# Performance work log

Hardware: AMD Instinct MI355X
Metric: run time of the kernel (lower is better)

## Reference

```python
import jax, jax.numpy as jnp
import numpy as np

BN_EPS = 1e-5

def _bn_relu(x, gamma, beta):
    # training-mode BatchNorm1d: biased batch stats over (B, N) per channel
    mean = x.mean(axis=(0, 2), keepdims=True)
    var = x.var(axis=(0, 2), keepdims=True)
    xn = (x - mean) * jax.lax.rsqrt(var + BN_EPS)
    return jax.nn.relu(xn * gamma[None, :, None] + beta[None, :, None])


def setup_inputs() -> dict:
    key = jax.random.key(0)
    ks = jax.random.split(key, 12)
    B, n1, n2, c1, c2 = 16, 4096, 1024, 128, 256
    in_ch, mlp = c1 + c2, [256, 128]
    xyz1 = jax.random.uniform(ks[0], (B, n1, 3), dtype=jnp.float32)
    xyz2 = jax.random.uniform(ks[1], (B, n2, 3), dtype=jnp.float32)
    feat1 = jax.random.normal(ks[2], (B, c1, n1), dtype=jnp.float32)
    feat2 = jax.random.normal(ks[3], (B, c2, n2), dtype=jnp.float32)
    # Conv1d(k=1) weights as (out, in) matrices; kaiming-ish scale
    w0 = jax.random.normal(ks[4], (mlp[0], in_ch), dtype=jnp.float32) / np.sqrt(in_ch)
    b0 = jnp.zeros((mlp[0],), jnp.float32)
    g0 = jnp.ones((mlp[0],), jnp.float32)
    be0 = jnp.zeros((mlp[0],), jnp.float32)
    w1 = jax.random.normal(ks[5], (mlp[1], mlp[0]), dtype=jnp.float32) / np.sqrt(mlp[0])
    b1 = jnp.zeros((mlp[1],), jnp.float32)
    g1 = jnp.ones((mlp[1],), jnp.float32)
    be1 = jnp.zeros((mlp[1],), jnp.float32)
    return {"xyz1": xyz1, "xyz2": xyz2, "feat1": feat1, "feat2": feat2,
            "w0": w0, "b0": b0, "g0": g0, "be0": be0,
            "w1": w1, "b1": b1, "g1": g1, "be1": be1}


def reference(xyz1, xyz2, feat1, feat2, w0, b0, g0, be0, w1, b1, g1, be1):
    # three_nn_interpolate: squared pairwise dists (B, n1, n2)
    d = jnp.sum((xyz1[:, :, None, :] - xyz2[:, None, :, :]) ** 2, axis=-1)
    neg_d3, idx3 = jax.lax.top_k(-d, 3)          # 3 smallest dists
    d3 = -neg_d3                                  # (B, n1, 3)
    w = 1.0 / (d3 + 1e-8)
    w = w / jnp.sum(w, axis=-1, keepdims=True)
    # gather feat2 at knn indices: (B, c2, n1, 3)
    gathered = jnp.take_along_axis(feat2[:, :, None, :], idx3[:, None, :, :], axis=3)
    interp = jnp.sum(gathered * w[:, None, :, :], axis=-1)  # (B, c2, n1)

    x = jnp.concatenate([feat1, interp], axis=1)            # (B, c1+c2, n1)
    x = _bn_relu(jnp.einsum('oc,bcn->bon', w0, x) + b0[None, :, None], g0, be0)
    x = _bn_relu(jnp.einsum('oc,bcn->bon', w1, x) + b1[None, :, None], g1, be1)
    return x
```

## Files before the change

kernel.cpp:

```cpp
#include <hip/hip_runtime.h>
#include <hip/hip_bf16.h>

typedef unsigned short u16;
typedef __attribute__((ext_vector_type(8))) __bf16 bf16x8;
typedef __attribute__((ext_vector_type(4))) float floatx4;

#define B_   16
#define N1_  4096
#define N2_  1024
#define C1_  128
#define C2_  256
#define CIN_ 384
#define CM_  256
#define CO_  128

__device__ __forceinline__ u16 f2bf(float f) {
  unsigned u = __float_as_uint(f);
  u = (u + 0x7fffu + ((u >> 16) & 1u)) >> 16;
  return (u16)u;
}
__device__ __forceinline__ float bf2f(u16 h) {
  return __uint_as_float(((unsigned)h) << 16);
}

union U128 { uint4 u; bf16x8 v; u16 s[8]; };

__device__ __forceinline__ bf16x8 ldfrag(const u16* p) {
  U128 x; x.u = *(const uint4*)p; return x.v;
}
__device__ __forceinline__ uint4 pack8(const u16* h) {
  uint4 u;
  u.x = (unsigned)h[0] | ((unsigned)h[1] << 16);
  u.y = (unsigned)h[2] | ((unsigned)h[3] << 16);
  u.z = (unsigned)h[4] | ((unsigned)h[5] << 16);
  u.w = (unsigned)h[6] | ((unsigned)h[7] << 16);
  return u;
}


__global__ __launch_bounds__(256) void mega_kernel(
    const float* __restrict__ xyz1, const float* __restrict__ xyz2,
    float* __restrict__ pd, int* __restrict__ pi,
    const float* __restrict__ w0, const float* __restrict__ w1,
    u16* __restrict__ w0b, u16* __restrict__ w1b,
    const float* __restrict__ feat2, u16* __restrict__ feat2Tb,
    const float* __restrict__ feat1, u16* __restrict__ xcatT)
{
  __shared__ __align__(16) float smem[64*133];
  int t = threadIdx.x;
  int id = blockIdx.x;
  if (id < 2048) {
    float4* sp = (float4*)smem;
    int xb = id & 15, b = (id >> 4) & 15, chunk = id >> 8;
    const float* p2 = xyz2 + ((size_t)b * N2_ + chunk * 128) * 3;
    if (t < 128) sp[t] = make_float4(p2[t*3], p2[t*3+1], p2[t*3+2], 0.f);
    __syncthreads();
    int i = xb * 256 + t;
    const float* p1 = xyz1 + ((size_t)b * N1_ + i) * 3;
    float x = p1[0], y = p1[1], z = p1[2];
    float d0 = 1e30f, d1 = 1e30f, d2 = 1e30f;
    int i0 = 0, i1 = 0, i2 = 0;
    int jb = chunk * 128;
    #pragma unroll 4
    for (int j = 0; j < 128; ++j) {
      float4 p = sp[j];
      float dx = x - p.x, dy = y - p.y, dz = z - p.z;
      float d = dx*dx + dy*dy + dz*dz;
      if (d < d2) {
        int jj = jb + j;
        if (d < d0)      { d2=d1; i2=i1; d1=d0; i1=i0; d0=d; i0=jj; }
        else if (d < d1) { d2=d1; i2=i1; d1=d;  i1=jj; }
        else             { d2=d;  i2=jj; }
      }
    }
    int o = chunk*65536 + b*4096 + i;
    pd[o] = d0; pd[o + 524288] = d1; pd[o + 1048576] = d2;
    pi[o] = i0; pi[o + 524288] = i1; pi[o + 1048576] = i2;
    return;
  }
  if (id < 2176) {
    int item = (id - 2048) * 256 + t;
    if (item < 12288) {
      int m = item / 48, kc = item % 48;
      const float* p = w0 + m * CIN_ + kc * 8;
      u16 h8[8];
      #pragma unroll
      for (int j = 0; j < 8; ++j) h8[j] = f2bf(p[j]);
      int mt = m >> 4, col = m & 15, kt = kc >> 2, quad = kc & 3;
      *(uint4*)(w0b + ((mt*12 + kt)*512 + (quad*16 + col)*8)) = pack8(h8);
    } else if (item < 16384) {
      int i2 = item - 12288;
      int m = i2 >> 5, kc = i2 & 31;
      const float* p = w1 + m * CM_ + kc * 8;
      u16 h8[8];
      #pragma unroll
      for (int j = 0; j < 8; ++j) h8[j] = f2bf(p[j]);
      int mt = m >> 4, col = m & 15, kt = kc >> 2, quad = kc & 3;
      *(uint4*)(w1b + ((mt*8 + kt)*512 + (quad*16 + col)*8)) = pack8(h8);
    }
    return;
  }
  if (id < 2432) {
    float (*sA2)[129] = (float(*)[129])smem;
    int idx = id - 2176;
    int b = idx >> 4, n0 = (idx & 15) * 64;
    #pragma unroll 1
    for (int h = 0; h < 2; ++h) {
      if (h) __syncthreads();
      #pragma unroll
      for (int j = 0; j < 8; ++j) {
        int flat4 = t + j * 256;
        int cl = flat4 >> 4, nn4 = (flat4 & 15) * 4;
        float4 v = *(const float4*)(feat2 + ((size_t)b*C2_ + h*128 + cl)*N2_ + n0 + nn4);
        sA2[nn4+0][cl] = v.x; sA2[nn4+1][cl] = v.y; sA2[nn4+2][cl] = v.z; sA2[nn4+3][cl] = v.w;
      }
      __syncthreads();
      int nn = t & 63, chunk = t >> 6;
      u16* dst = feat2Tb + ((size_t)b*N2_ + n0 + nn)*C2_ + h*128 + chunk*32;
      #pragma unroll
      for (int g = 0; g < 4; ++g) {
        u16 h8[8];
        #pragma unroll
        for (int j = 0; j < 8; ++j) h8[j] = f2bf(sA2[nn][chunk*32 + g*8 + j]);
        *(uint4*)(dst + g*8) = pack8(h8);
      }
    }
    return;
  }
  {
    float (*sA1)[133] = (float(*)[133])smem;
    int idx = id - 2432;
    int b = idx >> 6, n0 = (idx & 63) * 64;
    #pragma unroll
    for (int j = 0; j < 8; ++j) {
      int flat4 = t + j * 256;
      int c = flat4 >> 4, nn4 = (flat4 & 15) * 4;
      float4 v = *(const float4*)(feat1 + ((size_t)b*C1_ + c)*N1_ + n0 + nn4);
      sA1[nn4+0][c] = v.x; sA1[nn4+1][c] = v.y; sA1[nn4+2][c] = v.z; sA1[nn4+3][c] = v.w;
    }
    __syncthreads();
    int nn = t & 63, chunk = t >> 6;
    int n = n0 + nn, nt = n >> 4, col = n & 15;
    u16* tb = xcatT + ((size_t)b*256 + nt)*12*512;
    #pragma unroll
    for (int g = 0; g < 4; ++g) {
      int c0 = chunk*32 + g*8;
      u16 h8[8];
      #pragma unroll
      for (int j = 0; j < 8; ++j) h8[j] = f2bf(sA1[nn][c0 + j]);
      *(uint4*)(tb + (size_t)chunk*512 + (g*16 + col)*8) = pack8(h8);
    }
  }
}

__global__ __launch_bounds__(256) void merge_kernel(
    const float* __restrict__ pd, const int* __restrict__ pi,
    int* __restrict__ idx_out, float* __restrict__ w_out)
{
  int p = blockIdx.x * 256 + threadIdx.x;
  float d0 = 1e30f, d1 = 1e30f, d2 = 1e30f;
  int i0 = 0, i1 = 0, i2 = 0;
  #pragma unroll
  for (int c = 0; c < 8; ++c) {
    int o = c*65536 + p;
    #pragma unroll
    for (int k = 0; k < 3; ++k) {
      float d = pd[o + k*524288];
      int ix = pi[o + k*524288];
      bool c2 = d < d2, c1 = d < d1, c0 = d < d0;
      d2 = c1 ? d1 : (c2 ? d  : d2);
      i2 = c1 ? i1 : (c2 ? ix : i2);
      d1 = c0 ? d0 : (c1 ? d  : d1);
      i1 = c0 ? i0 : (c1 ? ix : i1);
      d0 = c0 ? d  : d0;
      i0 = c0 ? ix : i0;
    }
  }
  float w0 = 1.f/(d0+1e-8f), w1 = 1.f/(d1+1e-8f), w2 = 1.f/(d2+1e-8f);
  float inv = 1.f/(w0+w1+w2);
  idx_out[p]          = i0;
  idx_out[p +  65536] = i1;
  idx_out[p + 131072] = i2;
  w_out[p]            = w0*inv;
  w_out[p +  65536]   = w1*inv;
  w_out[p + 131072]   = w2*inv;
}

__global__ __launch_bounds__(256) void interp_kernel(
    const u16* __restrict__ feat2Tb,
    const int* __restrict__ idx_in, const float* __restrict__ w_in,
    u16* __restrict__ xcatT)
{
  int b = blockIdx.y;
  int t = threadIdx.x;
  int p0 = blockIdx.x * 64;
  int seg = t & 31;
  int pl  = t >> 5;
  #pragma unroll 2
  for (int pass = 0; pass < 8; ++pass) {
    int n = p0 + pass*8 + pl;
    int base = b*N1_ + n;
    int i0 = idx_in[base], i1 = idx_in[base + 65536], i2 = idx_in[base + 131072];
    float w0 = w_in[base], w1 = w_in[base + 65536], w2 = w_in[base + 131072];
    const u16* fb = feat2Tb + (size_t)b*N2_*C2_ + seg*8;
    U128 a, c, d;
    a.u = *(const uint4*)(fb + (size_t)i0*C2_);
    c.u = *(const uint4*)(fb + (size_t)i1*C2_);
    d.u = *(const uint4*)(fb + (size_t)i2*C2_);
    u16 h8[8];
    #pragma unroll
    for (int j = 0; j < 8; ++j)
      h8[j] = f2bf(w0*bf2f(a.s[j]) + w1*bf2f(c.s[j]) + w2*bf2f(d.s[j]));
    int nt = n >> 4, col = n & 15;
    int kt = 4 + (seg >> 2), quad = seg & 3;
    *(uint4*)(xcatT + (((size_t)b*256 + nt)*12 + kt)*512 + (quad*16 + col)*8) = pack8(h8);
  }
}

__global__ __launch_bounds__(256) void gemm1_mfma(
    const u16* __restrict__ xcatT, const u16* __restrict__ w0b,
    const float* __restrict__ b0p, u16* __restrict__ y0T,
    float* __restrict__ p0)
{
  __shared__ float ps[4][64][2];
  int t = threadIdx.x;
  int wave = t >> 6, lane = t & 63;
  int col = lane & 15, quad = lane >> 4;
  int wm = wave >> 1, wn = wave & 1;
  int b = blockIdx.y;
  int mtb = blockIdx.z*8 + wm*4;
  int ntb = blockIdx.x*8 + wn*4;

  const u16* ap = w0b + lane*8;
  const u16* bp = xcatT + ((size_t)(b*256 + ntb)*12)*512 + lane*8;

  floatx4 acc[4][4] = {};
  bf16x8 aA[4], aB[4], aC[4], aD[4], bA[4], bB[4], bC[4], bD[4];

#define G1_LDA(BUF, KT) { _Pragma("unroll") for (int i = 0; i < 4; ++i) \
    BUF[i] = ldfrag(ap + (size_t)((mtb+i)*12 + (KT))*512); }
#define G1_LDB(BUF, KT) { _Pragma("unroll") for (int i = 0; i < 4; ++i) \
    BUF[i] = ldfrag(bp + (size_t)(i*12 + (KT))*512); }
#define G1_MM(A_, B_) { _Pragma("unroll") for (int mt = 0; mt < 4; ++mt) \
    _Pragma("unroll") for (int nt = 0; nt < 4; ++nt) \
      acc[mt][nt] = __builtin_amdgcn_mfma_f32_16x16x32_bf16(A_[mt], B_[nt], acc[mt][nt], 0, 0, 0); }

  G1_LDA(aA,0);  G1_LDB(bA,0);
  G1_LDA(aB,1);  G1_LDB(bB,1);
  G1_LDA(aC,2);  G1_LDB(bC,2);
  G1_LDA(aD,3);  G1_LDB(bD,3);
  G1_MM(aA,bA);  G1_LDA(aA,4);  G1_LDB(bA,4);
  G1_MM(aB,bB);  G1_LDA(aB,5);  G1_LDB(bB,5);
  G1_MM(aC,bC);  G1_LDA(aC,6);  G1_LDB(bC,6);
  G1_MM(aD,bD);  G1_LDA(aD,7);  G1_LDB(bD,7);
  G1_MM(aA,bA);  G1_LDA(aA,8);  G1_LDB(bA,8);
  G1_MM(aB,bB);  G1_LDA(aB,9);  G1_LDB(bB,9);
  G1_MM(aC,bC);  G1_LDA(aC,10); G1_LDB(bC,10);
  G1_MM(aD,bD);  G1_LDA(aD,11); G1_LDB(bD,11);
  G1_MM(aA,bA);
  G1_MM(aB,bB);
  G1_MM(aC,bC);
  G1_MM(aD,bD);

  int m0 = blockIdx.z*128 + wm*64;
  #pragma unroll
  for (int mt = 0; mt < 4; ++mt) {
    float4 bias4 = *(const float4*)(b0p + m0 + mt*16 + quad*4);
    float bia[4] = {bias4.x, bias4.y, bias4.z, bias4.w};
    int kt_out = (m0 >> 5) + (mt >> 1);
    int quad_out = ((mt & 1) << 1) | (quad >> 1);
    int j0 = (quad & 1) * 4;
    float s[4] = {}, q[4] = {};
    #pragma unroll
    for (int nt = 0; nt < 4; ++nt) {
      int nt_g = ntb + nt;
      u16 h[4];
      #pragma unroll
      for (int r = 0; r < 4; ++r) {
        float v = acc[mt][nt][r] + bia[r];
        u16 hh = f2bf(v);
        float vr = bf2f(hh);
        h[r] = hh; s[r] += vr; q[r] += vr*vr;
      }
      *(ushort4*)(y0T + (((size_t)b*256 + nt_g)*8 + kt_out)*512 + (quad_out*16 + col)*8 + j0)
          = make_ushort4(h[0], h[1], h[2], h[3]);
    }
    #pragma unroll
    for (int r = 0; r < 4; ++r) {
      float ss = s[r], qq = q[r];
      #pragma unroll
      for (int msk = 1; msk < 16; msk <<= 1) { ss += __shfl_xor(ss, msk); qq += __shfl_xor(qq, msk); }
      if (col == 0) {
        ps[wave][mt*16 + quad*4 + r][0] = ss;
        ps[wave][mt*16 + quad*4 + r][1] = qq;
      }
    }
  }
  __syncthreads();
  {
    int c = t >> 1, k = t & 1;
    int wbase = (c >> 6) * 2, ch = c & 63;
    float v = ps[wbase][ch][k] + ps[wbase+1][ch][k];
    size_t l = (size_t)blockIdx.z*512 + blockIdx.y*32 + blockIdx.x;
    p0[l*256 + t] = v;
  }
}

__global__ __launch_bounds__(256) void stats_kernel(
    const float* __restrict__ p, const float* __restrict__ g,
    const float* __restrict__ be, float* __restrict__ scale,
    float* __restrict__ shift, int half_split, int nl)
{
  int c = blockIdx.x, t = threadIdx.x;
  size_t base = half_split ? ((size_t)(c >> 7) * 512 * 256 + (size_t)(c & 127) * 2)
                           : ((size_t)c * 2);
  float s = 0.f, q = 0.f;
  for (int i = 0; i < nl; ++i) {
    float2 v = *(const float2*)(p + base + (size_t)(t + i*256) * 256);
    s += v.x; q += v.y;
  }
  #pragma unroll
  for (int m = 1; m < 64; m <<= 1) { s += __shfl_xor(s, m); q += __shfl_xor(q, m); }
  __shared__ float2 red[4];
  if ((t & 63) == 0) red[t >> 6] = make_float2(s, q);
  __syncthreads();
  if (t == 0) {
    float ss = red[0].x + red[1].x + red[2].x + red[3].x;
    float qq = red[0].y + red[1].y + red[2].y + red[3].y;
    float mu  = ss * (1.f/65536.f);
    float var = qq * (1.f/65536.f) - mu*mu;
    float a = g[c] * rsqrtf(var + 1e-5f);
    scale[c] = a; shift[c] = be[c] - mu*a;
  }
}

__global__ __launch_bounds__(256) void gemm2_mfma(
    const u16* __restrict__ y0T, const u16* __restrict__ w1b,
    const float* __restrict__ b1p,
    const float* __restrict__ scale0, const float* __restrict__ shift0,
    float* __restrict__ out, float* __restrict__ p1)
{
  __shared__ float a0s[CM_], bb0s[CM_];
  __shared__ float ps[4][64][2];
  int t = threadIdx.x;
  a0s[t] = scale0[t]; bb0s[t] = shift0[t];
  __syncthreads();
  int wave = t >> 6, lane = t & 63;
  int col = lane & 15, quad = lane >> 4;
  int wm = wave >> 1, wn = wave & 1;
  int b = blockIdx.y;
  int mtb = wm*4;
  int ntb = blockIdx.x*8 + wn*4;

  const u16* ap = w1b + lane*8;
  const u16* bp = y0T + ((size_t)(b*256 + ntb)*8)*512 + lane*8;

  floatx4 acc[4][4] = {};
  bf16x8 aA[4], aB[4], aC[4];
  U128 rA[4], rB[4], rC[4];

#define G2_LDA(BUF, KT) { _Pragma("unroll") for (int i = 0; i < 4; ++i) \
    BUF[i] = ldfrag(ap + (size_t)((mtb+i)*8 + (KT))*512); }
#define G2_LDB(BUF, KT) { _Pragma("unroll") for (int i = 0; i < 4; ++i) \
    BUF[i].u = *(const uint4*)(bp + (size_t)(i*8 + (KT))*512); }
#define G2_BNMM(A_, R_, KT) { \
    int c0 = (KT)*32 + quad*8; \
    float av[8], bv[8]; \
    *(float4*)&av[0] = *(const float4*)&a0s[c0];  *(float4*)&av[4] = *(const float4*)&a0s[c0+4]; \
    *(float4*)&bv[0] = *(const float4*)&bb0s[c0]; *(float4*)&bv[4] = *(const float4*)&bb0s[c0+4]; \
    bf16x8 bfv[4]; \
    _Pragma("unroll") for (int j = 0; j < 4; ++j) { \
      u16 h8[8]; \
      _Pragma("unroll") for (int e = 0; e < 8; ++e) \
        h8[e] = f2bf(fmaxf(fmaf(bf2f(R_[j].s[e]), av[e], bv[e]), 0.f)); \
      U128 x_; x_.u = pack8(h8); bfv[j] = x_.v; } \
    _Pragma("unroll") for (int mt = 0; mt < 4; ++mt) \
    _Pragma("unroll") for (int nt = 0; nt < 4; ++nt) \
      acc[mt][nt] = __builtin_amdgcn_mfma_f32_16x16x32_bf16(A_[mt], bfv[nt], acc[mt][nt], 0, 0, 0); }

  G2_LDA(aA,0);  G2_LDB(rA,0);
  G2_LDA(aB,1);  G2_LDB(rB,1);
  G2_LDA(aC,2);  G2_LDB(rC,2);
  G2_BNMM(aA,rA,0);  G2_LDA(aA,3);  G2_LDB(rA,3);
  G2_BNMM(aB,rB,1);  G2_LDA(aB,4);  G2_LDB(rB,4);
  G2_BNMM(aC,rC,2);  G2_LDA(aC,5);  G2_LDB(rC,5);
  G2_BNMM(aA,rA,3);  G2_LDA(aA,6);  G2_LDB(rA,6);
  G2_BNMM(aB,rB,4);  G2_LDA(aB,7);  G2_LDB(rB,7);
  G2_BNMM(aC,rC,5);
  G2_BNMM(aA,rA,6);
  G2_BNMM(aB,rB,7);

  int m0 = wm*64;
  int n0 = blockIdx.x*128 + wn*64;
  #pragma unroll
  for (int mt = 0; mt < 4; ++mt) {
    float4 bias4 = *(const float4*)(b1p + m0 + mt*16 + quad*4);
    float bia[4] = {bias4.x, bias4.y, bias4.z, bias4.w};
    float s[4] = {}, q[4] = {};
    #pragma unroll
    for (int nt = 0; nt < 4; ++nt) {
      int n = n0 + nt*16 + col;
      #pragma unroll
      for (int r = 0; r < 4; ++r) {
        float v = acc[mt][nt][r] + bia[r];
        out[((size_t)b*CO_ + m0 + mt*16 + quad*4 + r)*N1_ + n] = v;
        s[r] += v; q[r] += v*v;
      }
    }
    #pragma unroll
    for (int r = 0; r < 4; ++r) {
      float ss = s[r], qq = q[r];
      #pragma unroll
      for (int msk = 1; msk < 16; msk <<= 1) { ss += __shfl_xor(ss, msk); qq += __shfl_xor(qq, msk); }
      if (col == 0) {
        ps[wave][mt*16 + quad*4 + r][0] = ss;
        ps[wave][mt*16 + quad*4 + r][1] = qq;
      }
    }
  }
  __syncthreads();
  {
    int c = t >> 1, k = t & 1;
    int wbase = (c >> 6) * 2, ch = c & 63;
    float v = ps[wbase][ch][k] + ps[wbase+1][ch][k];
    size_t l = (size_t)blockIdx.y*32 + blockIdx.x;
    p1[l*256 + t] = v;
  }
}

__global__ __launch_bounds__(256) void bnrelu_kernel(
    float* __restrict__ out, const float* __restrict__ scale1, const float* __restrict__ shift1)
{
  int idx = blockIdx.x * 256 + threadIdx.x;
  int c = (idx >> 10) & (CO_ - 1);
  float a = scale1[c];
  float bb = shift1[c];
  float4 v = ((const float4*)out)[idx];
  v.x = fmaxf(fmaf(v.x, a, bb), 0.f);
  v.y = fmaxf(fmaf(v.y, a, bb), 0.f);
  v.z = fmaxf(fmaf(v.z, a, bb), 0.f);
  v.w = fmaxf(fmaf(v.w, a, bb), 0.f);
  ((float4*)out)[idx] = v;
}

extern "C" void kernel_launch(void* const* d_in, const int* in_sizes, int n_in,
                              void* d_out, int out_size, void* d_ws, size_t ws_size,
                              hipStream_t stream)
{
  const float* xyz1  = (const float*)d_in[0];
  const float* xyz2  = (const float*)d_in[1];
  const float* feat1 = (const float*)d_in[2];
  const float* feat2 = (const float*)d_in[3];
  const float* w0    = (const float*)d_in[4];
  const float* b0    = (const float*)d_in[5];
  const float* g0    = (const float*)d_in[6];
  const float* be0   = (const float*)d_in[7];
  const float* w1    = (const float*)d_in[8];
  const float* b1    = (const float*)d_in[9];
  const float* g1    = (const float*)d_in[10];
  const float* be1   = (const float*)d_in[11];
  float* out = (float*)d_out;
  char* ws = (char*)d_ws;

  u16*   xcatT   = (u16*)ws;
  float* p1      = (float*)ws;
  u16*   y0T     = (u16*)(ws + 50331648);
  u16*   feat2Tb = (u16*)(ws + 50331648);
  float* knn_pd  = (float*)(ws + 58720256);
  int*   knn_pi  = (int*)(ws + 65011712);
  u16*   w0b     = (u16*)(ws + 83886080);
  u16*   w1b     = (u16*)(ws + 84082688);
  int*   idx_buf = (int*)(ws + 84148224);
  float* w_buf   = (float*)(ws + 84934656);
  float* p0      = (float*)(ws + 85721088);
  float* scale0  = (float*)(ws + 87293952);
  float* shift0  = scale0 + 256;
  float* scale1  = scale0 + 512;
  float* shift1  = scale0 + 640;

  mega_kernel  <<<3456,           256, 0, stream>>>(xyz1, xyz2, knn_pd, knn_pi, w0, w1,
                                                    w0b, w1b, feat2, feat2Tb, feat1, xcatT);
  merge_kernel <<<256,            256, 0, stream>>>(knn_pd, knn_pi, idx_buf, w_buf);
  interp_kernel<<<dim3(64,16),    256, 0, stream>>>(feat2Tb, idx_buf, w_buf, xcatT);
  gemm1_mfma   <<<dim3(32,16,2),  256, 0, stream>>>(xcatT, w0b, b0, y0T, p0);
  stats_kernel <<<256,            256, 0, stream>>>(p0, g0, be0, scale0, shift0, 1, 2);
  gemm2_mfma   <<<dim3(32,16),    256, 0, stream>>>(y0T, w1b, b1, scale0, shift0, out, p1);
  stats_kernel <<<128,            256, 0, stream>>>(p1, g1, be1, scale1, shift1, 0, 2);
  bnrelu_kernel<<<8192,           256, 0, stream>>>(out, scale1, shift1);
}
```

Before: 248.1 us.

## Split KNN into two chunks and fuse top-3 merge into interp kernel

The KNN search now splits the 1024 candidate points into 2 chunks of 512 instead of 8 chunks of 128. This shrinks the partial-result buffers and the number of KNN blocks. The separate merge kernel is removed: the first 64 threads of each interp block merge the two partial top-3 lists, compute the inverse-distance weights and stage them in shared memory. The gemm1 prefetch pipeline also drops from four register buffers to three, which lowers register pressure at the cost of a shallower prefetch. The trade-off is less block-level parallelism in the KNN phase, which now has 512 blocks instead of 2048.

```diff
diff --git a/kernel.cpp b/kernel.cpp
--- a/kernel.cpp
+++ b/kernel.cpp
@@ -49,20 +49,22 @@
   __shared__ __align__(16) float smem[64*133];
   int t = threadIdx.x;
   int id = blockIdx.x;
-  if (id < 2048) {
+  if (id < 512) {
     float4* sp = (float4*)smem;
     int xb = id & 15, b = (id >> 4) & 15, chunk = id >> 8;
-    const float* p2 = xyz2 + ((size_t)b * N2_ + chunk * 128) * 3;
-    if (t < 128) sp[t] = make_float4(p2[t*3], p2[t*3+1], p2[t*3+2], 0.f);
+    const float* p2 = xyz2 + ((size_t)b * N2_ + chunk * 512) * 3;
+    #pragma unroll
+    for (int l = t; l < 512; l += 256)
+      sp[l] = make_float4(p2[l*3], p2[l*3+1], p2[l*3+2], 0.f);
     __syncthreads();
     int i = xb * 256 + t;
     const float* p1 = xyz1 + ((size_t)b * N1_ + i) * 3;
     float x = p1[0], y = p1[1], z = p1[2];
     float d0 = 1e30f, d1 = 1e30f, d2 = 1e30f;
     int i0 = 0, i1 = 0, i2 = 0;
-    int jb = chunk * 128;
+    int jb = chunk * 512;
     #pragma unroll 4
-    for (int j = 0; j < 128; ++j) {
+    for (int j = 0; j < 512; ++j) {
       float4 p = sp[j];
       float dx = x - p.x, dy = y - p.y, dz = z - p.z;
       float d = dx*dx + dy*dy + dz*dz;
@@ -74,12 +76,12 @@
       }
     }
     int o = chunk*65536 + b*4096 + i;
-    pd[o] = d0; pd[o + 524288] = d1; pd[o + 1048576] = d2;
-    pi[o] = i0; pi[o + 524288] = i1; pi[o + 1048576] = i2;
+    pd[o] = d0; pd[o + 131072] = d1; pd[o + 262144] = d2;
+    pi[o] = i0; pi[o + 131072] = i1; pi[o + 262144] = i2;
     return;
   }
-  if (id < 2176) {
-    int item = (id - 2048) * 256 + t;
+  if (id < 640) {
+    int item = (id - 512) * 256 + t;
     if (item < 12288) {
       int m = item / 48, kc = item % 48;
       const float* p = w0 + m * CIN_ + kc * 8;
@@ -100,9 +102,9 @@
     }
     return;
   }
-  if (id < 2432) {
+  if (id < 896) {
     float (*sA2)[129] = (float(*)[129])smem;
-    int idx = id - 2176;
+    int idx = id - 640;
     int b = idx >> 4, n0 = (idx & 15) * 64;
     #pragma unroll 1
     for (int h = 0; h < 2; ++h) {
@@ -129,7 +131,7 @@
   }
   {
     float (*sA1)[133] = (float(*)[133])smem;
-    int idx = id - 2432;
+    int idx = id - 896;
     int b = idx >> 6, n0 = (idx & 63) * 64;
     #pragma unroll
     for (int j = 0; j < 8; ++j) {
@@ -153,55 +155,50 @@
   }
 }
 
-__global__ __launch_bounds__(256) void merge_kernel(
-    const float* __restrict__ pd, const int* __restrict__ pi,
-    int* __restrict__ idx_out, float* __restrict__ w_out)
-{
-  int p = blockIdx.x * 256 + threadIdx.x;
-  float d0 = 1e30f, d1 = 1e30f, d2 = 1e30f;
-  int i0 = 0, i1 = 0, i2 = 0;
-  #pragma unroll
-  for (int c = 0; c < 8; ++c) {
-    int o = c*65536 + p;
-    #pragma unroll
-    for (int k = 0; k < 3; ++k) {
-      float d = pd[o + k*524288];
-      int ix = pi[o + k*524288];
-      bool c2 = d < d2, c1 = d < d1, c0 = d < d0;
-      d2 = c1 ? d1 : (c2 ? d  : d2);
-      i2 = c1 ? i1 : (c2 ? ix : i2);
-      d1 = c0 ? d0 : (c1 ? d  : d1);
-      i1 = c0 ? i0 : (c1 ? ix : i1);
-      d0 = c0 ? d  : d0;
-      i0 = c0 ? ix : i0;
-    }
-  }
-  float w0 = 1.f/(d0+1e-8f), w1 = 1.f/(d1+1e-8f), w2 = 1.f/(d2+1e-8f);
-  float inv = 1.f/(w0+w1+w2);
-  idx_out[p]          = i0;
-  idx_out[p +  65536] = i1;
-  idx_out[p + 131072] = i2;
-  w_out[p]            = w0*inv;
-  w_out[p +  65536]   = w1*inv;
-  w_out[p + 131072]   = w2*inv;
-}
-
 __global__ __launch_bounds__(256) void interp_kernel(
     const u16* __restrict__ feat2Tb,
-    const int* __restrict__ idx_in, const float* __restrict__ w_in,
+    const float* __restrict__ pd, const int* __restrict__ pi,
     u16* __restrict__ xcatT)
 {
+  __shared__ int   sidx[3][64];
+  __shared__ float sw[3][64];
   int b = blockIdx.y;
   int t = threadIdx.x;
   int p0 = blockIdx.x * 64;
+  if (t < 64) {
+    int p = b*4096 + p0 + t;
+    float d0 = 1e30f, d1 = 1e30f, d2 = 1e30f;
+    int i0 = 0, i1 = 0, i2 = 0;
+    #pragma unroll
+    for (int c = 0; c < 2; ++c) {
+      int o = c*65536 + p;
+      #pragma unroll
+      for (int k = 0; k < 3; ++k) {
+        float d = pd[o + k*131072];
+        int ix = pi[o + k*131072];
+        bool c2 = d < d2, c1 = d < d1, c0 = d < d0;
+        d2 = c1 ? d1 : (c2 ? d  : d2);
+        i2 = c1 ? i1 : (c2 ? ix : i2);
+        d1 = c0 ? d0 : (c1 ? d  : d1);
+        i1 = c0 ? i0 : (c1 ? ix : i1);
+        d0 = c0 ? d  : d0;
+        i0 = c0 ? ix : i0;
+      }
+    }
+    float w0 = 1.f/(d0+1e-8f), w1 = 1.f/(d1+1e-8f), w2 = 1.f/(d2+1e-8f);
+    float inv = 1.f/(w0+w1+w2);
+    sidx[0][t] = i0; sidx[1][t] = i1; sidx[2][t] = i2;
+    sw[0][t] = w0*inv; sw[1][t] = w1*inv; sw[2][t] = w2*inv;
+  }
+  __syncthreads();
   int seg = t & 31;
   int pl  = t >> 5;
   #pragma unroll 2
   for (int pass = 0; pass < 8; ++pass) {
-    int n = p0 + pass*8 + pl;
-    int base = b*N1_ + n;
-    int i0 = idx_in[base], i1 = idx_in[base + 65536], i2 = idx_in[base + 131072];
-    float w0 = w_in[base], w1 = w_in[base + 65536], w2 = w_in[base + 131072];
+    int nl = pass*8 + pl;
+    int n = p0 + nl;
+    int i0 = sidx[0][nl], i1 = sidx[1][nl], i2 = sidx[2][nl];
+    float w0 = sw[0][nl], w1 = sw[1][nl], w2 = sw[2][nl];
     const u16* fb = feat2Tb + (size_t)b*N2_*C2_ + seg*8;
     U128 a, c, d;
     a.u = *(const uint4*)(fb + (size_t)i0*C2_);
@@ -235,7 +232,7 @@
   const u16* bp = xcatT + ((size_t)(b*256 + ntb)*12)*512 + lane*8;
 
   floatx4 acc[4][4] = {};
-  bf16x8 aA[4], aB[4], aC[4], aD[4], bA[4], bB[4], bC[4], bD[4];
+  bf16x8 aA[4], aB[4], aC[4], bA[4], bB[4], bC[4];
 
 #define G1_LDA(BUF, KT) { _Pragma("unroll") for (int i = 0; i < 4; ++i) \
     BUF[i] = ldfrag(ap + (size_t)((mtb+i)*12 + (KT))*512); }
@@ -248,19 +245,18 @@
   G1_LDA(aA,0);  G1_LDB(bA,0);
   G1_LDA(aB,1);  G1_LDB(bB,1);
   G1_LDA(aC,2);  G1_LDB(bC,2);
-  G1_LDA(aD,3);  G1_LDB(bD,3);
-  G1_MM(aA,bA);  G1_LDA(aA,4);  G1_LDB(bA,4);
-  G1_MM(aB,bB);  G1_LDA(aB,5);  G1_LDB(bB,5);
-  G1_MM(aC,bC);  G1_LDA(aC,6);  G1_LDB(bC,6);
-  G1_MM(aD,bD);  G1_LDA(aD,7);  G1_LDB(bD,7);
-  G1_MM(aA,bA);  G1_LDA(aA,8);  G1_LDB(bA,8);
-  G1_MM(aB,bB);  G1_LDA(aB,9);  G1_LDB(bB,9);
-  G1_MM(aC,bC);  G1_LDA(aC,10); G1_LDB(bC,10);
-  G1_MM(aD,bD);  G1_LDA(aD,11); G1_LDB(bD,11);
+  G1_MM(aA,bA);  G1_LDA(aA,3);  G1_LDB(bA,3);
+  G1_MM(aB,bB);  G1_LDA(aB,4);  G1_LDB(bB,4);
+  G1_MM(aC,bC);  G1_LDA(aC,5);  G1_LDB(bC,5);
+  G1_MM(aA,bA);  G1_LDA(aA,6);  G1_LDB(bA,6);
+  G1_MM(aB,bB);  G1_LDA(aB,7);  G1_LDB(bB,7);
+  G1_MM(aC,bC);  G1_LDA(aC,8);  G1_LDB(bC,8);
+  G1_MM(aA,bA);  G1_LDA(aA,9);  G1_LDB(bA,9);
+  G1_MM(aB,bB);  G1_LDA(aB,10); G1_LDB(bB,10);
+  G1_MM(aC,bC);  G1_LDA(aC,11); G1_LDB(bC,11);
   G1_MM(aA,bA);
   G1_MM(aB,bB);
   G1_MM(aC,bC);
-  G1_MM(aD,bD);
 
   int m0 = blockIdx.z*128 + wm*64;
   #pragma unroll
@@ -470,18 +466,15 @@
   int*   knn_pi  = (int*)(ws + 65011712);
   u16*   w0b     = (u16*)(ws + 83886080);
   u16*   w1b     = (u16*)(ws + 84082688);
-  int*   idx_buf = (int*)(ws + 84148224);
-  float* w_buf   = (float*)(ws + 84934656);
   float* p0      = (float*)(ws + 85721088);
   float* scale0  = (float*)(ws + 87293952);
   float* shift0  = scale0 + 256;
   float* scale1  = scale0 + 512;
   float* shift1  = scale0 + 640;
 
-  mega_kernel  <<<3456,           256, 0, stream>>>(xyz1, xyz2, knn_pd, knn_pi, w0, w1,
+  mega_kernel  <<<1920,           256, 0, stream>>>(xyz1, xyz2, knn_pd, knn_pi, w0, w1,
                                                     w0b, w1b, feat2, feat2Tb, feat1, xcatT);
-  merge_kernel <<<256,            256, 0, stream>>>(knn_pd, knn_pi, idx_buf, w_buf);
-  interp_kernel<<<dim3(64,16),    256, 0, stream>>>(feat2Tb, idx_buf, w_buf, xcatT);
+  interp_kernel<<<dim3(64,16),    256, 0, stream>>>(feat2Tb, knn_pd, knn_pi, xcatT);
   gemm1_mfma   <<<dim3(32,16,2),  256, 0, stream>>>(xcatT, w0b, b0, y0T, p0);
   stats_kernel <<<256,            256, 0, stream>>>(p0, g0, be0, scale0, shift0, 1, 2);
   gemm2_mfma   <<<dim3(32,16),    256, 0, stream>>>(y0T, w1b, b1, scale0, shift0, out, p1);
```

Result: slower. 253.2 us (+2.0%).
